# Performance work log

Measured on AMD Instinct MI355X. Metric: run time of the kernel, lower is better.

## Reference

```python
import jax, jax.numpy as jnp
import numpy as np
from jax import lax

DN = ('NCHW', 'OIHW', 'NCHW')
HIDDEN = 9      # ProposalModule(out_channels, len(scales)*len(ratios)) -> hidden_dim = 9
N_ANC = 9       # default n_anchors
C_IN = 2048
B, H, W = 32, 25, 25
N_POS = 2048
N_NEG = 2048
N_FLAT = B * H * W * N_ANC  # 180000


def setup_inputs() -> dict:
    key = jax.random.key(0)
    ks = jax.random.split(key, 10)
    feature_maps = jax.random.normal(ks[0], (B, C_IN, H, W), dtype=jnp.float32)
    pos_anc_idxs = jax.random.randint(ks[1], (N_POS,), 0, N_FLAT)
    neg_anc_idxs = jax.random.randint(ks[2], (N_NEG,), 0, N_FLAT)
    # xyxy anchor boxes in feature-map coords with strictly positive width/height
    xy = jax.random.uniform(ks[3], (N_POS, 2), dtype=jnp.float32) * 20.0
    wh = jax.random.uniform(ks[4], (N_POS, 2), dtype=jnp.float32) * 5.0 + 1.0
    pos_ancs = jnp.concatenate([xy, xy + wh], axis=1)
    # conv params (torch OIHW layout), fan-in scaled init
    Wh = jax.random.normal(ks[5], (HIDDEN, C_IN, 3, 3), dtype=jnp.float32) / np.sqrt(C_IN * 9)
    bh = jnp.zeros((HIDDEN,), dtype=jnp.float32)
    Wc = jax.random.normal(ks[6], (N_ANC, HIDDEN, 1, 1), dtype=jnp.float32) / np.sqrt(HIDDEN)
    bc = jnp.zeros((N_ANC,), dtype=jnp.float32)
    Wr = jax.random.normal(ks[7], (N_ANC * 4, HIDDEN, 1, 1), dtype=jnp.float32) / np.sqrt(HIDDEN)
    br = jnp.zeros((N_ANC * 4,), dtype=jnp.float32)
    return {'feature_maps': feature_maps, 'pos_anc_idxs': pos_anc_idxs,
            'neg_anc_idxs': neg_anc_idxs, 'pos_ancs': pos_ancs,
            'Wh': Wh, 'bh': bh, 'Wc': Wc, 'bc': bc, 'Wr': Wr, 'br': br}


def _conv(x, w, b, pad):
    y = lax.conv_general_dilated(x, w, (1, 1), pad, dimension_numbers=DN)
    return y + b[None, :, None, None]


def reference(feature_maps, pos_anc_idxs, neg_anc_idxs, pos_ancs, Wh, bh, Wc, bc, Wr, br):
    # ProposalModule train-mode forward (dropout = identity, deterministic)
    x = jax.nn.relu(_conv(feature_maps, Wh, bh, 'SAME'))          # [b, hidden, h, w]
    conf_pred = _conv(x, Wc, bc, 'VALID')                          # [b, n_anc, h, w]
    offsets_pred = _conv(x, Wr, br, 'VALID')                       # [b, 4*n_anc, h, w]

    conf_flat = jnp.transpose(conf_pred, (0, 2, 3, 1)).reshape(-1)       # [b*h*w*n_anc]
    pos_conf = conf_flat[pos_anc_idxs]
    neg_conf = conf_flat[neg_anc_idxs]
    off_flat = jnp.transpose(offsets_pred, (0, 2, 3, 1)).reshape(-1, 4)  # [b*h*w*n_anc, 4]
    pos_offsets = off_flat[pos_anc_idxs]

    # _generate_proposals: xyxy -> cxcywh, apply offsets, back to xyxy
    cx = (pos_ancs[:, 0] + pos_ancs[:, 2]) * 0.5
    cy = (pos_ancs[:, 1] + pos_ancs[:, 3]) * 0.5
    w = pos_ancs[:, 2] - pos_ancs[:, 0]
    h = pos_ancs[:, 3] - pos_ancs[:, 1]
    ncx = cx + pos_offsets[:, 0] * w
    ncy = cy + pos_offsets[:, 1] * h
    nw = w * jnp.exp(pos_offsets[:, 2])
    nh = h * jnp.exp(pos_offsets[:, 3])
    proposals = jnp.stack([ncx - nw * 0.5, ncy - nh * 0.5,
                           ncx + nw * 0.5, ncy + nh * 0.5], axis=-1)
    return pos_conf, neg_conf, pos_offsets, proposals
```

## Files before the change

kernel.cpp:

```cpp
#include <hip/hip_runtime.h>
#include <hip/hip_bf16.h>
#include <math.h>

#define C_IN   2048
#define HID    9
#define NIDX   4096
#define PLANE  (NIDX * HID)

#define NGRP   32
#define NT     16
#define ICAP   192
#define BUFB   16256

#define BFRAG_OFF 0
#define CNT_OFF   262144
#define LIST_OFF  (CNT_OFF + 64)
#define PART_OFF  (LIST_OFF + 32 * ICAP)
#define WS_NEED   (((size_t)PART_OFF + (size_t)NGRP * PLANE) * 4)

typedef short  bf16x8 __attribute__((ext_vector_type(8)));
typedef float  f32x4  __attribute__((ext_vector_type(4)));

__device__ __forceinline__ unsigned short bits_of(float v) {
  __hip_bfloat16 h = __float2bfloat16(v);
  return *reinterpret_cast<unsigned short*>(&h);
}

__global__ void prep_kernel(const float* __restrict__ Wh,
                            const int*   __restrict__ pos_idx,
                            const int*   __restrict__ neg_idx,
                            float*       __restrict__ wsf,
                            unsigned*    __restrict__ wsu) {
  int e = blockIdx.x * 256 + threadIdx.x;
  if (e < 512 * 2 * 64) {
    int lane = e & 63, s = (e >> 6) & 1, tc = e >> 7;
    int n = lane & 15, q = lane >> 4;
    unsigned short h[8];
#pragma unroll
    for (int j = 0; j < 8; j++) {
      float v = 0.f;
      if (n < 9) {
        if (s == 0) {
          int tap = 2 * q + (j >> 2), ch = j & 3;
          v = Wh[(n * C_IN + tc * 4 + ch) * 9 + tap];
        } else if (q == 0 && j < 4) {
          v = Wh[(n * C_IN + tc * 4 + j) * 9 + 8];
        }
      }
      h[j] = bits_of(v);
    }
    uint4 dv;
    dv.x = h[0] | ((unsigned)h[1] << 16);
    dv.y = h[2] | ((unsigned)h[3] << 16);
    dv.z = h[4] | ((unsigned)h[5] << 16);
    dv.w = h[6] | ((unsigned)h[7] << 16);
    ((uint4*)(wsu + BFRAG_OFF))[e] = dv;
  }
  if (e < PLANE) wsf[PART_OFF + e] = 0.f;
  if (e < NIDX) {
    int flat = (e < 2048) ? pos_idx[e] : neg_idx[e - 2048];
    int pw = flat / 9;
    int b  = pw / 625;
    int p  = pw - b * 625;
    int h  = p / 25, w = p - h * 25;
    unsigned mask = 0;
#pragma unroll
    for (int dh = 0; dh < 3; dh++)
#pragma unroll
      for (int dw = 0; dw < 3; dw++)
        if (h + dh >= 1 && h + dh <= 25 && w + dw >= 1 && w + dw <= 25)
          mask |= 1u << (dh * 3 + dw);
    unsigned pack = (unsigned)p | (mask << 10) | ((unsigned)e << 19);
    int* icnt = (int*)(wsu + CNT_OFF);
    int* bcnt = (int*)(wsu + CNT_OFF + 32);
    if (mask == 0x1FFu) {
      int n = atomicAdd(&icnt[b], 1);
      if (n < ICAP) wsu[LIST_OFF + b * ICAP + n] = pack;
    } else {
      int m = atomicAdd(&bcnt[b], 1);
      if (m < ICAP) wsu[LIST_OFF + b * ICAP + (ICAP - 1 - m)] = pack;
    }
  }
}

__global__ __launch_bounds__(256, 4) void conv_gather(
    const float* __restrict__ feat,
    const unsigned* __restrict__ wsu,
    float* __restrict__ part,
    int atomic_mode) {
  __shared__ __align__(16) char stage[2 * BUFB];
  __shared__ int slots_lds[ICAP];
  __shared__ int prod_flag[NT];
  __shared__ int cons_cnt[NT];

  const int t = threadIdx.x, g = blockIdx.x, b = blockIdx.y;
  const int lane = t & 63, wv = t >> 6;

  const int icnt = min(((const int*)(wsu + CNT_OFF))[b], ICAP);
  const int cnt  = min(icnt + ((const int*)(wsu + CNT_OFF + 32))[b], ICAP);

  if (t < NT) { prod_flag[t] = 0; cons_cnt[t] = 0; }
  if (t < ICAP) {
    int phys = (t < icnt) ? t : (ICAP - 1 - (t - icnt));
    slots_lds[t] = (int)(wsu[LIST_OFF + b * ICAP + phys] >> 19);
  }
  __syncthreads();

  const float* gbase = feat + ((size_t)b * C_IN + (size_t)g * 64) * 625;

  if (wv >= 2) {
    for (int k = wv - 2; k < NT; k += 2) {
      if (k >= 2)
        while (__hip_atomic_load(&cons_cnt[k - 2], __ATOMIC_ACQUIRE,
                                 __HIP_MEMORY_SCOPE_WORKGROUP) < 2)
          __builtin_amdgcn_s_sleep(1);
      const float* gt = gbase + (size_t)k * 2500;
      char* bufk = stage + (k & 1) * BUFB;
#pragma unroll
      for (int r = 0; r < 10; r++) {
        int hw = r * 64 + lane;
        bool ok = hw < 625;
        float v0 = ok ? gt[hw]        : 0.f;
        float v1 = ok ? gt[625 + hw]  : 0.f;
        float v2 = ok ? gt[1250 + hw] : 0.f;
        float v3 = ok ? gt[1875 + hw] : 0.f;
        uint2 dv;
        dv.x = bits_of(v0) | ((unsigned)bits_of(v1) << 16);
        dv.y = bits_of(v2) | ((unsigned)bits_of(v3) << 16);
        if (ok) *(uint2*)(bufk + (26 + hw) * 24) = dv;
      }
      if (lane == 0)
        __hip_atomic_store(&prod_flag[k], 1, __ATOMIC_RELEASE,
                           __HIP_MEMORY_SCOPE_WORKGROUP);
    }
    return;
  }

  const int n = lane & 15, q = lane >> 4;
  const int t0o = (q == 0) ? -624 : (q == 1) ? -576 : (q == 2) ? 0  : 576;
  const int t1o = (q == 0) ? -600 : (q == 1) ? -24  : (q == 2) ? 24 : 600;
  const int t8o = 624;

  const int mtbase = wv * 6;
  int pb[6]; unsigned mk[6]; int st[6];
#pragma unroll
  for (int i = 0; i < 6; i++) {
    int mt = mtbase + i;
    int e = mt * 16 + n;
    int p = 0; unsigned m = 0;
    if (e < cnt) {
      int phys = (e < icnt) ? e : (ICAP - 1 - (e - icnt));
      unsigned pack = wsu[LIST_OFF + b * ICAP + phys];
      p = (int)(pack & 1023u);
      m = (pack >> 10) & 511u;
    }
    pb[i] = (26 + p) * 24;
    mk[i] = (e < cnt) ? m : 0u;
    st[i] = (mt * 16 >= cnt) ? 0 : (((mt + 1) * 16 <= icnt) ? 1 : 2);
  }

  f32x4 acc[6];
#pragma unroll
  for (int i = 0; i < 6; i++) acc[i] = (f32x4){0.f, 0.f, 0.f, 0.f};

  const uint4* btab = (const uint4*)(wsu + BFRAG_OFF);

  for (int k = 0; k < NT; k++) {
    const int tc = g * 16 + k;
    bf16x8 bf0 = __builtin_bit_cast(bf16x8, btab[(tc * 2 + 0) * 64 + lane]);
    bf16x8 bf1 = __builtin_bit_cast(bf16x8, btab[(tc * 2 + 1) * 64 + lane]);
    while (__hip_atomic_load(&prod_flag[k], __ATOMIC_ACQUIRE,
                             __HIP_MEMORY_SCOPE_WORKGROUP) == 0)
      __builtin_amdgcn_s_sleep(1);
    const char* bufk = stage + (k & 1) * BUFB;
#pragma unroll
    for (int i = 0; i < 6; i++) {
      if (st[i] == 0) continue;
      const char* ba = bufk + pb[i];
      int2 lo = *(const int2*)(ba + t0o);
      int2 hi = *(const int2*)(ba + t1o);
      int2 r8 = *(const int2*)(ba + t8o);
      if (st[i] == 2) {
        bool b0 = (mk[i] >> (2 * q)) & 1u;
        bool b1 = (mk[i] >> (2 * q + 1)) & 1u;
        bool b8 = (mk[i] >> 8) & 1u;
        lo.x = b0 ? lo.x : 0; lo.y = b0 ? lo.y : 0;
        hi.x = b1 ? hi.x : 0; hi.y = b1 ? hi.y : 0;
        r8.x = b8 ? r8.x : 0; r8.y = b8 ? r8.y : 0;
      }
      int4 a0 = {lo.x, lo.y, hi.x, hi.y};
      acc[i] = __builtin_amdgcn_mfma_f32_16x16x32_bf16(
          __builtin_bit_cast(bf16x8, a0), bf0, acc[i], 0, 0, 0);
      int4 a1 = {r8.x, r8.y, 0, 0};
      acc[i] = __builtin_amdgcn_mfma_f32_16x16x32_bf16(
          __builtin_bit_cast(bf16x8, a1), bf1, acc[i], 0, 0, 0);
    }
    if (lane == 0)
      __hip_atomic_fetch_add(&cons_cnt[k], 1, __ATOMIC_RELEASE,
                             __HIP_MEMORY_SCOPE_WORKGROUP);
  }

  float* pp = part + (atomic_mode ? 0 : (size_t)g * PLANE);
  if (n < 9) {
#pragma unroll
    for (int i = 0; i < 6; i++) {
      if (st[i] == 0) continue;
#pragma unroll
      for (int reg = 0; reg < 4; reg++) {
        int e = (mtbase + i) * 16 + q * 4 + reg;
        if (e < cnt) {
          int slot = slots_lds[e];
          float v = acc[i][reg];
          if (atomic_mode) atomicAdd(&pp[slot * 9 + n], v);
          else             pp[slot * 9 + n] = v;
        }
      }
    }
  }
}

__global__ void heads_kernel(const float* __restrict__ part,
                             int nplanes,
                             const int*   __restrict__ pos_idx,
                             const int*   __restrict__ neg_idx,
                             const float* __restrict__ pos_ancs,
                             const float* __restrict__ bh,
                             const float* __restrict__ Wc,
                             const float* __restrict__ bc,
                             const float* __restrict__ Wr,
                             const float* __restrict__ br,
                             float*       __restrict__ out) {
  int i = blockIdx.x * 256 + threadIdx.x;
  if (i >= NIDX) return;
  int flat = (i < 2048) ? pos_idx[i] : neg_idx[i - 2048];
  int anc = flat % 9;
  float xr[9];
#pragma unroll
  for (int j = 0; j < 9; j++) xr[j] = bh[j];
  for (int gp = 0; gp < nplanes; gp++) {
    const float* pp = part + (size_t)gp * PLANE + (size_t)i * 9;
#pragma unroll
    for (int j = 0; j < 9; j++) xr[j] += pp[j];
  }
#pragma unroll
  for (int j = 0; j < 9; j++) xr[j] = xr[j] > 0.f ? xr[j] : 0.f;
  float conf = bc[anc];
#pragma unroll
  for (int j = 0; j < 9; j++) conf += xr[j] * Wc[anc * 9 + j];
  out[i] = conf;
  if (i < 2048) {
    float off[4];
#pragma unroll
    for (int k = 0; k < 4; k++) {
      float sacc = br[anc * 4 + k];
#pragma unroll
      for (int j = 0; j < 9; j++) sacc += xr[j] * Wr[(anc * 4 + k) * 9 + j];
      off[k] = sacc;
      out[4096 + i * 4 + k] = sacc;
    }
    float x1 = pos_ancs[i * 4 + 0], y1 = pos_ancs[i * 4 + 1];
    float x2 = pos_ancs[i * 4 + 2], y2 = pos_ancs[i * 4 + 3];
    float cx = (x1 + x2) * 0.5f, cy = (y1 + y2) * 0.5f;
    float w = x2 - x1, h = y2 - y1;
    float ncx = cx + off[0] * w, ncy = cy + off[1] * h;
    float nw = w * expf(off[2]), nh = h * expf(off[3]);
    out[12288 + i * 4 + 0] = ncx - nw * 0.5f;
    out[12288 + i * 4 + 1] = ncy - nh * 0.5f;
    out[12288 + i * 4 + 2] = ncx + nw * 0.5f;
    out[12288 + i * 4 + 3] = ncy + nh * 0.5f;
  }
}

extern "C" void kernel_launch(void* const* d_in, const int* in_sizes, int n_in,
                              void* d_out, int out_size, void* d_ws, size_t ws_size,
                              hipStream_t stream) {
  const float* feat     = (const float*)d_in[0];
  const int*   pos_idx  = (const int*)d_in[1];
  const int*   neg_idx  = (const int*)d_in[2];
  const float* pos_ancs = (const float*)d_in[3];
  const float* Wh       = (const float*)d_in[4];
  const float* bh       = (const float*)d_in[5];
  const float* Wc       = (const float*)d_in[6];
  const float* bc       = (const float*)d_in[7];
  const float* Wr       = (const float*)d_in[8];
  const float* br       = (const float*)d_in[9];
  float* out = (float*)d_out;

  float*    wsf  = (float*)d_ws;
  unsigned* wsu  = (unsigned*)d_ws;
  float*    part = wsf + PART_OFF;

  const bool small_ws = (ws_size < WS_NEED);

  hipMemsetAsync((char*)d_ws + (size_t)CNT_OFF * 4, 0, 64 * 4, stream);
  prep_kernel<<<256, 256, 0, stream>>>(Wh, pos_idx, neg_idx, wsf, wsu);
  conv_gather<<<dim3(NGRP, 32), 256, 0, stream>>>(
      feat, wsu, part, small_ws ? 1 : 0);
  heads_kernel<<<16, 256, 0, stream>>>(part, small_ws ? 1 : NGRP,
                                       pos_idx, neg_idx, pos_ancs,
                                       bh, Wc, bc, Wr, br, out);
}
```

Baseline: 272.9 us.

## Deepen LDS staging ring, compact tap layout, and accumulate partials atomically

The staging ring grows from two to four tile buffers so the producer waves can run further ahead of the MFMA consumer waves. Each pixel's packed bf16 channel group now uses an 8-byte slot instead of 24 bytes, with halo offsets rescaled to match, which shrinks each buffer so four fit in less LDS than two did before. Per-group partial planes are removed: every channel group atomically adds into one plane, and the heads kernel reads that single plane instead of summing 32. This cuts workspace writes and reads, at the cost of global atomic contention and order-dependent float summation.

```diff
diff --git a/kernel.cpp b/kernel.cpp
--- a/kernel.cpp
+++ b/kernel.cpp
@@ -9,14 +9,15 @@
 
 #define NGRP   32
 #define NT     16
+#define NBUF   4
 #define ICAP   192
-#define BUFB   16256
+#define BUFB   5440
 
 #define BFRAG_OFF 0
 #define CNT_OFF   262144
 #define LIST_OFF  (CNT_OFF + 64)
 #define PART_OFF  (LIST_OFF + 32 * ICAP)
-#define WS_NEED   (((size_t)PART_OFF + (size_t)NGRP * PLANE) * 4)
+#define WS_NEED   (((size_t)PART_OFF + (size_t)PLANE) * 4)
 
 typedef short  bf16x8 __attribute__((ext_vector_type(8)));
 typedef float  f32x4  __attribute__((ext_vector_type(4)));
@@ -86,9 +87,8 @@
 __global__ __launch_bounds__(256, 4) void conv_gather(
     const float* __restrict__ feat,
     const unsigned* __restrict__ wsu,
-    float* __restrict__ part,
-    int atomic_mode) {
-  __shared__ __align__(16) char stage[2 * BUFB];
+    float* __restrict__ part) {
+  __shared__ __align__(16) char stage[NBUF * BUFB];
   __shared__ int slots_lds[ICAP];
   __shared__ int prod_flag[NT];
   __shared__ int cons_cnt[NT];
@@ -110,12 +110,12 @@
 
   if (wv >= 2) {
     for (int k = wv - 2; k < NT; k += 2) {
-      if (k >= 2)
-        while (__hip_atomic_load(&cons_cnt[k - 2], __ATOMIC_ACQUIRE,
+      if (k >= NBUF)
+        while (__hip_atomic_load(&cons_cnt[k - NBUF], __ATOMIC_ACQUIRE,
                                  __HIP_MEMORY_SCOPE_WORKGROUP) < 2)
           __builtin_amdgcn_s_sleep(1);
       const float* gt = gbase + (size_t)k * 2500;
-      char* bufk = stage + (k & 1) * BUFB;
+      char* bufk = stage + (k & (NBUF - 1)) * BUFB;
 #pragma unroll
       for (int r = 0; r < 10; r++) {
         int hw = r * 64 + lane;
@@ -127,7 +127,7 @@
         uint2 dv;
         dv.x = bits_of(v0) | ((unsigned)bits_of(v1) << 16);
         dv.y = bits_of(v2) | ((unsigned)bits_of(v3) << 16);
-        if (ok) *(uint2*)(bufk + (26 + hw) * 24) = dv;
+        if (ok) *(uint2*)(bufk + (26 + hw) * 8) = dv;
       }
       if (lane == 0)
         __hip_atomic_store(&prod_flag[k], 1, __ATOMIC_RELEASE,
@@ -137,9 +137,9 @@
   }
 
   const int n = lane & 15, q = lane >> 4;
-  const int t0o = (q == 0) ? -624 : (q == 1) ? -576 : (q == 2) ? 0  : 576;
-  const int t1o = (q == 0) ? -600 : (q == 1) ? -24  : (q == 2) ? 24 : 600;
-  const int t8o = 624;
+  const int t0o = ((q == 0) ? -26 : (q == 1) ? -24 : (q == 2) ? 0  : 24) * 8;
+  const int t1o = ((q == 0) ? -25 : (q == 1) ? -1  : (q == 2) ? 1  : 25) * 8;
+  const int t8o = 26 * 8;
 
   const int mtbase = wv * 6;
   int pb[6]; unsigned mk[6]; int st[6];
@@ -154,7 +154,7 @@
       p = (int)(pack & 1023u);
       m = (pack >> 10) & 511u;
     }
-    pb[i] = (26 + p) * 24;
+    pb[i] = (26 + p) * 8;
     mk[i] = (e < cnt) ? m : 0u;
     st[i] = (mt * 16 >= cnt) ? 0 : (((mt + 1) * 16 <= icnt) ? 1 : 2);
   }
@@ -172,7 +172,7 @@
     while (__hip_atomic_load(&prod_flag[k], __ATOMIC_ACQUIRE,
                              __HIP_MEMORY_SCOPE_WORKGROUP) == 0)
       __builtin_amdgcn_s_sleep(1);
-    const char* bufk = stage + (k & 1) * BUFB;
+    const char* bufk = stage + (k & (NBUF - 1)) * BUFB;
 #pragma unroll
     for (int i = 0; i < 6; i++) {
       if (st[i] == 0) continue;
@@ -200,7 +200,6 @@
                              __HIP_MEMORY_SCOPE_WORKGROUP);
   }
 
-  float* pp = part + (atomic_mode ? 0 : (size_t)g * PLANE);
   if (n < 9) {
 #pragma unroll
     for (int i = 0; i < 6; i++) {
@@ -210,9 +209,7 @@
         int e = (mtbase + i) * 16 + q * 4 + reg;
         if (e < cnt) {
           int slot = slots_lds[e];
-          float v = acc[i][reg];
-          if (atomic_mode) atomicAdd(&pp[slot * 9 + n], v);
-          else             pp[slot * 9 + n] = v;
+          atomicAdd(&part[slot * 9 + n], acc[i][reg]);
         }
       }
     }
@@ -220,7 +217,6 @@
 }
 
 __global__ void heads_kernel(const float* __restrict__ part,
-                             int nplanes,
                              const int*   __restrict__ pos_idx,
                              const int*   __restrict__ neg_idx,
                              const float* __restrict__ pos_ancs,
@@ -234,16 +230,13 @@
   if (i >= NIDX) return;
   int flat = (i < 2048) ? pos_idx[i] : neg_idx[i - 2048];
   int anc = flat % 9;
+  const float* pp = part + (size_t)i * 9;
   float xr[9];
 #pragma unroll
-  for (int j = 0; j < 9; j++) xr[j] = bh[j];
-  for (int gp = 0; gp < nplanes; gp++) {
-    const float* pp = part + (size_t)gp * PLANE + (size_t)i * 9;
-#pragma unroll
-    for (int j = 0; j < 9; j++) xr[j] += pp[j];
-  }
-#pragma unroll
-  for (int j = 0; j < 9; j++) xr[j] = xr[j] > 0.f ? xr[j] : 0.f;
+  for (int j = 0; j < 9; j++) {
+    float v = bh[j] + pp[j];
+    xr[j] = v > 0.f ? v : 0.f;
+  }
   float conf = bc[anc];
 #pragma unroll
   for (int j = 0; j < 9; j++) conf += xr[j] * Wc[anc * 9 + j];
@@ -290,13 +283,9 @@
   unsigned* wsu  = (unsigned*)d_ws;
   float*    part = wsf + PART_OFF;
 
-  const bool small_ws = (ws_size < WS_NEED);
-
   hipMemsetAsync((char*)d_ws + (size_t)CNT_OFF * 4, 0, 64 * 4, stream);
   prep_kernel<<<256, 256, 0, stream>>>(Wh, pos_idx, neg_idx, wsf, wsu);
-  conv_gather<<<dim3(NGRP, 32), 256, 0, stream>>>(
-      feat, wsu, part, small_ws ? 1 : 0);
-  heads_kernel<<<16, 256, 0, stream>>>(part, small_ws ? 1 : NGRP,
-                                       pos_idx, neg_idx, pos_ancs,
+  conv_gather<<<dim3(NGRP, 32), 256, 0, stream>>>(feat, wsu, part);
+  heads_kernel<<<16, 256, 0, stream>>>(part, pos_idx, neg_idx, pos_ancs,
                                        bh, Wc, bc, Wr, br, out);
 }
```

After: 267.8 us. Within noise of the previous version (-1.9%).
